# Kernel tuning notes

Hardware: AMD Instinct MI355X
Metric: run time of the kernel (lower is better)

Reference implementation:

```python
import jax, jax.numpy as jnp
import numpy as np
from jax import lax

D_MODEL, D_STATE, DT_RANK = 2048, 16, 128
B_SZ, SEQLEN = 4, 2048


def setup_inputs() -> dict:
    key = jax.random.key(0)
    ks = jax.random.split(key, 8)
    dt_init_std = DT_RANK ** (-0.5)
    return {
        "hidden_states": jax.random.normal(ks[0], (B_SZ, SEQLEN, D_MODEL), jnp.float32),
        "x_proj_weight": jax.random.normal(ks[1], (DT_RANK + 2 * D_STATE, D_MODEL), jnp.float32) * (D_MODEL ** -0.5),
        "dt_proj_weight": jax.random.uniform(ks[2], (D_MODEL, DT_RANK), jnp.float32, -dt_init_std, dt_init_std),
        "dt_proj_bias": jax.random.normal(ks[3], (D_MODEL,), jnp.float32) * 0.5 - 4.0,  # ~inv-softplus of small dt
        "A_log": jnp.log(jax.random.uniform(ks[4], (D_MODEL, D_STATE), jnp.float32) * D_STATE + 1.0),
        "D": jax.random.uniform(ks[5], (D_MODEL,), jnp.float32) * 0.8,
        "out_proj_weight": jax.random.normal(ks[6], (D_MODEL, D_MODEL), jnp.float32) * (D_MODEL ** -0.5),
        "out_proj_bias": jax.random.normal(ks[7], (D_MODEL,), jnp.float32) * 0.02,
    }


def _s6_forward(hidden_states, x_proj_weight, dt_proj_weight, dt_proj_bias,
                A_log, D, out_proj_weight, out_proj_bias):
    b, L, d = hidden_states.shape
    W = x_proj_weight.T                                   # [d, r+2n]
    r = dt_proj_weight.shape[1]
    n = (W.shape[1] - r) // 2
    dt_down = W[:, :r]                                    # [d, r]
    WB = W[:, r:r + n]                                    # [d, n]
    WC = W[:, r + n:]                                     # [d, n]

    Bm = jnp.einsum('bld,dn->bln', hidden_states, WB)     # [b, L, n]
    Cm = jnp.einsum('bld,dn->bln', hidden_states, WC)     # [b, L, n]
    dt_w = dt_proj_weight @ dt_down.T                     # [d, d] fused dt projection
    dt = jnp.einsum('bld,ed->ble', hidden_states, dt_w)   # [b, L, d]

    A = -jnp.exp(A_log)                                   # [d, n]
    delta = jax.nn.softplus(dt + dt_proj_bias)            # [b, L, d]

    def step(h, inp):
        delta_t, B_t, C_t, x_t = inp                      # [b,d],[b,n],[b,n],[b,d]
        dA = jnp.exp(delta_t[..., None] * A)              # [b, d, n]
        h = h * dA + (delta_t * x_t)[..., None] * B_t[:, None, :]
        y_t = jnp.einsum('bdn,bn->bd', h, C_t)
        return h, y_t

    h0 = jnp.zeros((b, d, n), hidden_states.dtype)
    xs = (delta.transpose(1, 0, 2), Bm.transpose(1, 0, 2),
          Cm.transpose(1, 0, 2), hidden_states.transpose(1, 0, 2))
    _, ys = lax.scan(step, h0, xs)                        # ys: [L, b, d]
    y = ys.transpose(1, 0, 2)                             # [b, L, d]

    out = jax.nn.relu(y @ out_proj_weight.T + out_proj_bias)
    out = out + D * hidden_states                         # theory mode: D applied post-relu
    return out


def reference(hidden_states, x_proj_weight, dt_proj_weight, dt_proj_bias,
              A_log, D, out_proj_weight, out_proj_bias):
    return _s6_forward(hidden_states, x_proj_weight, dt_proj_weight, dt_proj_bias,
                       A_log, D, out_proj_weight, out_proj_bias)
```

## Files before the change

kernel.cpp:

```cpp
#include <hip/hip_runtime.h>
#include <hip/hip_bf16.h>
#include <stdint.h>

#define D_MODEL 2048
#define D_STATE 16
#define DT_RANK 128
#define B_SZ 4
#define SEQLEN 2048
#define MROWS (B_SZ * SEQLEN)
#define NPROJ (DT_RANK + 2 * D_STATE)
#define NCHUNK 32
#define CHUNK (SEQLEN / NCHUNK)

typedef short bf16x8 __attribute__((ext_vector_type(8)));
typedef unsigned short ushort8 __attribute__((ext_vector_type(8)));
typedef float f32x4 __attribute__((ext_vector_type(4)));

__device__ __forceinline__ unsigned short f2bf(float f) {
  union { float f; uint32_t u; } a; a.f = f;
  uint32_t u = a.u;
  u += 0x7fffu + ((u >> 16) & 1u);
  return (unsigned short)(u >> 16);
}
__device__ __forceinline__ float bf2f(unsigned short h) {
  union { uint32_t u; float f; } a; a.u = ((uint32_t)h) << 16;
  return a.f;
}

__device__ __forceinline__ void async16(const void* g, void* l) {
  __builtin_amdgcn_global_load_lds((const __attribute__((address_space(1))) void*)g,
                                   (__attribute__((address_space(3))) void*)(uintptr_t)l,
                                   16, 0, 0);
}

template<int BM, int BN, int WMv, int WNv, bool A_BF, bool B_BF, int EPI>
__global__ __launch_bounds__(256)
void gemm_nt(const float* __restrict__ Af, const unsigned short* __restrict__ Ab,
             const float* __restrict__ Bf, const unsigned short* __restrict__ Bb,
             int K,
             float* __restrict__ outf, unsigned short* __restrict__ outb,
             const float* __restrict__ bias, const float* __restrict__ Dvec,
             const float* __restrict__ hsres)
{
  constexpr int TM = BM / WMv, TN = BN / WNv;
  constexpr int FM = TM / 16, FN = TN / 16;
  __shared__ char smem[(BM + BN) * 64];
  char* smA = smem;
  char* smB = smem + BM * 64;

  const int tid  = threadIdx.x;
  const int lane = tid & 63;
  const int wid  = tid >> 6;
  const int wm   = wid / WNv, wn = wid % WNv;
  const int wrow = wm * TM,  wcol = wn * TN;
  const int row0 = blockIdx.x * BM;
  const int col0 = blockIdx.y * BN;

  f32x4 acc[FM][FN] = {};

  for (int k0 = 0; k0 < K; k0 += 32) {
    if constexpr (A_BF) {
      #pragma unroll
      for (int it = 0; it < (BM * 4) / 256; ++it) {
        int c = it * 256 + tid;
        const char* g = (const char*)(Ab + (size_t)(row0 + (c >> 2)) * K + k0) + (c & 3) * 16;
        async16(g, smA + it * 4096 + (tid & ~63) * 16);
      }
    } else {
      constexpr int CH = BM * 4;
      #pragma unroll
      for (int it = 0; it < (CH + 255) / 256; ++it) {
        int c = it * 256 + tid;
        if ((CH % 256 == 0) || (c < CH)) {
          const float* g = Af + (size_t)(row0 + (c >> 2)) * K + k0 + (c & 3) * 8;
          float4 u = *reinterpret_cast<const float4*>(g);
          float4 v = *reinterpret_cast<const float4*>(g + 4);
          ushort8 p;
          p[0] = f2bf(u.x); p[1] = f2bf(u.y); p[2] = f2bf(u.z); p[3] = f2bf(u.w);
          p[4] = f2bf(v.x); p[5] = f2bf(v.y); p[6] = f2bf(v.z); p[7] = f2bf(v.w);
          *reinterpret_cast<ushort8*>(smA + c * 16) = p;
        }
      }
    }
    if constexpr (B_BF) {
      #pragma unroll
      for (int it = 0; it < (BN * 4) / 256; ++it) {
        int c = it * 256 + tid;
        const char* g = (const char*)(Bb + (size_t)(col0 + (c >> 2)) * K + k0) + (c & 3) * 16;
        async16(g, smB + it * 4096 + (tid & ~63) * 16);
      }
    } else {
      constexpr int CH = BN * 4;
      #pragma unroll
      for (int it = 0; it < (CH + 255) / 256; ++it) {
        int c = it * 256 + tid;
        if ((CH % 256 == 0) || (c < CH)) {
          const float* g = Bf + (size_t)(col0 + (c >> 2)) * K + k0 + (c & 3) * 8;
          float4 u = *reinterpret_cast<const float4*>(g);
          float4 v = *reinterpret_cast<const float4*>(g + 4);
          ushort8 p;
          p[0] = f2bf(u.x); p[1] = f2bf(u.y); p[2] = f2bf(u.z); p[3] = f2bf(u.w);
          p[4] = f2bf(v.x); p[5] = f2bf(v.y); p[6] = f2bf(v.z); p[7] = f2bf(v.w);
          *reinterpret_cast<ushort8*>(smB + c * 16) = p;
        }
      }
    }
    __syncthreads();

    bf16x8 a[FM], b[FN];
    const int kb = (lane >> 4) * 16;
    #pragma unroll
    for (int i = 0; i < FM; ++i)
      a[i] = *reinterpret_cast<const bf16x8*>(smA + (wrow + i * 16 + (lane & 15)) * 64 + kb);
    #pragma unroll
    for (int j = 0; j < FN; ++j)
      b[j] = *reinterpret_cast<const bf16x8*>(smB + (wcol + j * 16 + (lane & 15)) * 64 + kb);
    #pragma unroll
    for (int i = 0; i < FM; ++i)
      #pragma unroll
      for (int j = 0; j < FN; ++j)
        acc[i][j] = __builtin_amdgcn_mfma_f32_16x16x32_bf16(a[i], b[j], acc[i][j], 0, 0, 0);
    __syncthreads();
  }

  #pragma unroll
  for (int i = 0; i < FM; ++i) {
    #pragma unroll
    for (int j = 0; j < FN; ++j) {
      #pragma unroll
      for (int r = 0; r < 4; ++r) {
        int grow = row0 + wrow + i * 16 + ((lane >> 4) * 4) + r;
        int gcol = col0 + wcol + j * 16 + (lane & 15);
        float v = acc[i][j][r];
        if constexpr (EPI == 0) {
          outf[(size_t)grow * NPROJ + gcol] = v;
          if (gcol < DT_RANK) outb[(size_t)grow * DT_RANK + gcol] = f2bf(v);
        } else if constexpr (EPI == 1) {
          float s = v + bias[gcol];
          s = (s > 20.f) ? s : log1pf(__expf(s));
          outb[(size_t)grow * D_MODEL + gcol] = f2bf(s);
        } else {
          float s = fmaxf(v + bias[gcol], 0.f)
                    + Dvec[gcol] * hsres[(size_t)grow * D_MODEL + gcol];
          outf[(size_t)grow * D_MODEL + gcol] = s;
        }
      }
    }
  }
}

template<bool P2>
__global__ __launch_bounds__(256)
void scan_chunk(const unsigned short* __restrict__ delta,
                const float* __restrict__ hs,
                const float* __restrict__ xdbc,
                const float* __restrict__ A_log,
                float* __restrict__ Ssum, float* __restrict__ Hloc,
                const float* __restrict__ Hinit,
                unsigned short* __restrict__ y)
{
  const int b  = blockIdx.z;
  const int c  = blockIdx.y;
  const int d  = blockIdx.x * 256 + threadIdx.x;
  const int t0 = c * CHUNK;
  __shared__ float Bs[CHUNK][16];
  __shared__ float Cs[P2 ? CHUNK : 1][16];

  {
    int tt = threadIdx.x >> 2, nn = (threadIdx.x & 3) * 4;
    const float* src = xdbc + (size_t)(b * SEQLEN + t0 + tt) * NPROJ + DT_RANK;
    *reinterpret_cast<float4*>(&Bs[tt][nn]) = *reinterpret_cast<const float4*>(src + nn);
    if constexpr (P2)
      *reinterpret_cast<float4*>(&Cs[tt][nn]) = *reinterpret_cast<const float4*>(src + D_STATE + nn);
  }

  float A[16], h[16];
  #pragma unroll
  for (int n = 0; n < 16; ++n) A[n] = -__expf(A_log[d * 16 + n]);
  const size_t hoff = ((size_t)((b * NCHUNK + c) * D_MODEL) + d) * 16;
  if constexpr (P2) {
    #pragma unroll
    for (int n = 0; n < 16; ++n) h[n] = Hinit[hoff + n];
  } else {
    #pragma unroll
    for (int n = 0; n < 16; ++n) h[n] = 0.f;
  }
  __syncthreads();

  float S = 0.f;
  const size_t rbase = (size_t)(b * SEQLEN + t0) * D_MODEL + d;
  #pragma unroll 2
  for (int t = 0; t < CHUNK; ++t) {
    float dlt = bf2f(delta[rbase + (size_t)t * D_MODEL]);
    float x   = hs[rbase + (size_t)t * D_MODEL];
    float dx  = dlt * x;
    S += dlt;
    float yv = 0.f;
    #pragma unroll
    for (int n = 0; n < 16; ++n) {
      float dA = __expf(dlt * A[n]);
      h[n] = fmaf(h[n], dA, dx * Bs[t][n]);
      if constexpr (P2) yv = fmaf(h[n], Cs[t][n], yv);
    }
    if constexpr (P2) y[rbase + (size_t)t * D_MODEL] = f2bf(yv);
  }

  if constexpr (!P2) {
    Ssum[(size_t)((b * NCHUNK + c) * D_MODEL) + d] = S;
    #pragma unroll
    for (int n = 0; n < 16; ++n) Hloc[hoff + n] = h[n];
  }
}

__global__ __launch_bounds__(256)
void scan_prop(const float* __restrict__ A_log, const float* __restrict__ Ssum,
               const float* __restrict__ Hloc, float* __restrict__ Hinit)
{
  int idx = blockIdx.x * 256 + threadIdx.x;
  int n = idx & 15, d = (idx >> 4) & (D_MODEL - 1), b = idx >> 15;
  float A = -__expf(A_log[d * D_STATE + n]);
  float H = 0.f;
  for (int c = 0; c < NCHUNK; ++c) {
    size_t off = ((size_t)((b * NCHUNK + c) * D_MODEL) + d) * 16 + n;
    Hinit[off] = H;
    float P = __expf(A * Ssum[(size_t)((b * NCHUNK + c) * D_MODEL) + d]);
    H = fmaf(H, P, Hloc[off]);
  }
}

__global__ __launch_bounds__(256)
void cast_kernel(const float* __restrict__ in, unsigned short* __restrict__ out)
{
  int i = (blockIdx.x * 256 + threadIdx.x) * 8;
  float4 u = *reinterpret_cast<const float4*>(in + i);
  float4 v = *reinterpret_cast<const float4*>(in + i + 4);
  ushort8 p;
  p[0] = f2bf(u.x); p[1] = f2bf(u.y); p[2] = f2bf(u.z); p[3] = f2bf(u.w);
  p[4] = f2bf(v.x); p[5] = f2bf(v.y); p[6] = f2bf(v.z); p[7] = f2bf(v.w);
  *reinterpret_cast<ushort8*>(out + i) = p;
}

extern "C" void kernel_launch(void* const* d_in, const int* in_sizes, int n_in,
                              void* d_out, int out_size, void* d_ws, size_t ws_size,
                              hipStream_t stream)
{
  const float* hs   = (const float*)d_in[0];
  const float* xpw  = (const float*)d_in[1];
  const float* dtw  = (const float*)d_in[2];
  const float* dtb  = (const float*)d_in[3];
  const float* Alog = (const float*)d_in[4];
  const float* Dv   = (const float*)d_in[5];
  const float* opw  = (const float*)d_in[6];
  const float* opb  = (const float*)d_in[7];
  float* out = (float*)d_out;

  char* ws = (char*)d_ws;
  float*          xdbc  = (float*)(ws);
  unsigned short* dtmp  = (unsigned short*)(ws + 5242880);
  unsigned short* delta = (unsigned short*)(ws + 7340032);
  unsigned short* ybf   = (unsigned short*)(ws + 40894464);
  unsigned short* w3b   = (unsigned short*)(ws + 74448896);
  float*          Hloc  = (float*)(ws + 82837504);
  float*          Hinit = (float*)(ws + 99614720);
  float*          Ssum  = (float*)(ws + 116391936);

  cast_kernel<<<dim3((D_MODEL * D_MODEL) / (256 * 8)), 256, 0, stream>>>(opw, w3b);

  gemm_nt<64, 32, 2, 2, false, false, 0>
      <<<dim3(MROWS / 64, NPROJ / 32), 256, 0, stream>>>(
      hs, nullptr, xpw, nullptr, D_MODEL, xdbc, dtmp, nullptr, nullptr, nullptr);

  gemm_nt<128, 128, 2, 2, true, false, 1>
      <<<dim3(MROWS / 128, D_MODEL / 128), 256, 0, stream>>>(
      nullptr, dtmp, dtw, nullptr, DT_RANK, nullptr, delta, dtb, nullptr, nullptr);

  scan_chunk<false><<<dim3(D_MODEL / 256, NCHUNK, B_SZ), 256, 0, stream>>>(
      delta, hs, xdbc, Alog, Ssum, Hloc, nullptr, nullptr);
  scan_prop<<<dim3((B_SZ * D_MODEL * D_STATE) / 256), 256, 0, stream>>>(
      Alog, Ssum, Hloc, Hinit);
  scan_chunk<true><<<dim3(D_MODEL / 256, NCHUNK, B_SZ), 256, 0, stream>>>(
      delta, hs, xdbc, Alog, nullptr, nullptr, Hinit, ybf);

  gemm_nt<128, 128, 2, 2, true, true, 2>
      <<<dim3(MROWS / 128, D_MODEL / 128), 256, 0, stream>>>(
      nullptr, ybf, nullptr, w3b, D_MODEL, out, nullptr, opb, Dv, hs);

  (void)in_sizes; (void)n_in; (void)out_size; (void)ws_size;
}
```

Before: 491.6 us.

## Add triple-buffered 256x128 async-LDS GEMM for dt and out projections

Adds a new gemm_big kernel with 512 threads, 256x128 tiles, K-step 64, a three-stage async global-to-LDS pipeline, an XOR-swizzled LDS layout and a grouped block-index swizzle. It is used for the dt-projection and out-projection GEMMs. The x_proj and dt_proj weights are now pre-cast to bf16, and the x_proj GEMM becomes a single 160-wide column tile that loads bf16 B through async loads. The aim is to overlap memory latency with MFMA work and cut LDS bank conflicts, at the cost of more LDS per block and extra cast launches.

```diff
diff --git a/kernel.cpp b/kernel.cpp
--- a/kernel.cpp
+++ b/kernel.cpp
@@ -33,14 +33,119 @@
                                    16, 0, 0);
 }
 
+template<int EPI>
+__global__ __launch_bounds__(512, 2)
+void gemm_big(const unsigned short* __restrict__ A, const unsigned short* __restrict__ B,
+              int K,
+              float* __restrict__ outf, unsigned short* __restrict__ outb,
+              const float* __restrict__ bias, const float* __restrict__ Dvec,
+              const float* __restrict__ hsres)
+{
+  __shared__ char lds[3 * 49152];
+
+  const int tid  = threadIdx.x;
+  const int lane = tid & 63;
+  const int wid  = tid >> 6;
+  const int wrow = (wid >> 1) * 64;
+  const int wcol = (wid & 1) * 64;
+  const int nwg = gridDim.x;
+  const int cpx = nwg >> 3;
+  const int swz = (blockIdx.x & 7) * cpx + (blockIdx.x >> 3);
+  const int mb  = swz >> 4;
+  const int nb  = swz & 15;
+  const int row0 = mb * 256;
+  const int col0 = nb * 128;
+
+  const int nt = K >> 6;
+
+  auto stage_tile = [&](int t, int q) {
+    const int k0 = t * 64;
+    char* bufA = lds + q * 49152;
+    char* bufB = bufA + 32768;
+    #pragma unroll
+    for (int it = 0; it < 4; ++it) {
+      int c = it * 512 + tid;
+      int gc = c ^ ((c >> 3) & 7);
+      const char* g = (const char*)(A + (size_t)(row0 + (gc >> 3)) * K + k0) + (gc & 7) * 16;
+      async16(g, bufA + (c & ~63) * 16);
+    }
+    #pragma unroll
+    for (int it = 0; it < 2; ++it) {
+      int c = it * 512 + tid;
+      int gc = c ^ ((c >> 3) & 7);
+      const char* g = (const char*)(B + (size_t)(col0 + (gc >> 3)) * K + k0) + (gc & 7) * 16;
+      async16(g, bufB + (c & ~63) * 16);
+    }
+  };
+
+  f32x4 acc[4][4] = {};
+
+  stage_tile(0, 0);
+  stage_tile(1, 1);
+
+  for (int t = 0; t < nt; ++t) {
+    if (t < nt - 1) asm volatile("s_waitcnt vmcnt(6)" ::: "memory");
+    else            asm volatile("s_waitcnt vmcnt(0)" ::: "memory");
+    __builtin_amdgcn_s_barrier();
+    if (t + 2 < nt) stage_tile(t + 2, (t + 2) % 3);
+
+    const char* bufA = lds + (t % 3) * 49152;
+    const char* bufB = bufA + 32768;
+    #pragma unroll
+    for (int kk = 0; kk < 2; ++kk) {
+      bf16x8 a[4], b[4];
+      #pragma unroll
+      for (int i = 0; i < 4; ++i) {
+        int r = wrow + i * 16 + (lane & 15);
+        int byt = r * 128 + kk * 64 + ((lane >> 4) * 16);
+        a[i] = *reinterpret_cast<const bf16x8*>(bufA + (byt ^ ((r & 7) << 4)));
+      }
+      #pragma unroll
+      for (int j = 0; j < 4; ++j) {
+        int r = wcol + j * 16 + (lane & 15);
+        int byt = r * 128 + kk * 64 + ((lane >> 4) * 16);
+        b[j] = *reinterpret_cast<const bf16x8*>(bufB + (byt ^ ((r & 7) << 4)));
+      }
+      __builtin_amdgcn_s_setprio(1);
+      #pragma unroll
+      for (int i = 0; i < 4; ++i)
+        #pragma unroll
+        for (int j = 0; j < 4; ++j)
+          acc[i][j] = __builtin_amdgcn_mfma_f32_16x16x32_bf16(a[i], b[j], acc[i][j], 0, 0, 0);
+      __builtin_amdgcn_s_setprio(0);
+    }
+  }
+
+  #pragma unroll
+  for (int i = 0; i < 4; ++i) {
+    #pragma unroll
+    for (int j = 0; j < 4; ++j) {
+      #pragma unroll
+      for (int r = 0; r < 4; ++r) {
+        int grow = row0 + wrow + i * 16 + ((lane >> 4) * 4) + r;
+        int gcol = col0 + wcol + j * 16 + (lane & 15);
+        float v = acc[i][j][r];
+        if constexpr (EPI == 1) {
+          float s = v + bias[gcol];
+          s = (s > 20.f) ? s : log1pf(__expf(s));
+          outb[(size_t)grow * D_MODEL + gcol] = f2bf(s);
+        } else {
+          float s = fmaxf(v + bias[gcol], 0.f)
+                    + Dvec[gcol] * hsres[(size_t)grow * D_MODEL + gcol];
+          outf[(size_t)grow * D_MODEL + gcol] = s;
+        }
+      }
+    }
+  }
+}
+
 template<int BM, int BN, int WMv, int WNv, bool A_BF, bool B_BF, int EPI>
 __global__ __launch_bounds__(256)
 void gemm_nt(const float* __restrict__ Af, const unsigned short* __restrict__ Ab,
              const float* __restrict__ Bf, const unsigned short* __restrict__ Bb,
              int K,
              float* __restrict__ outf, unsigned short* __restrict__ outb,
-             const float* __restrict__ bias, const float* __restrict__ Dvec,
-             const float* __restrict__ hsres)
+             const float* __restrict__ bias)
 {
   constexpr int TM = BM / WMv, TN = BN / WNv;
   constexpr int FM = TM / 16, FN = TN / 16;
@@ -59,49 +164,45 @@
   f32x4 acc[FM][FN] = {};
 
   for (int k0 = 0; k0 < K; k0 += 32) {
-    if constexpr (A_BF) {
-      #pragma unroll
-      for (int it = 0; it < (BM * 4) / 256; ++it) {
-        int c = it * 256 + tid;
-        const char* g = (const char*)(Ab + (size_t)(row0 + (c >> 2)) * K + k0) + (c & 3) * 16;
-        async16(g, smA + it * 4096 + (tid & ~63) * 16);
-      }
-    } else {
+    {
       constexpr int CH = BM * 4;
       #pragma unroll
       for (int it = 0; it < (CH + 255) / 256; ++it) {
         int c = it * 256 + tid;
         if ((CH % 256 == 0) || (c < CH)) {
-          const float* g = Af + (size_t)(row0 + (c >> 2)) * K + k0 + (c & 3) * 8;
-          float4 u = *reinterpret_cast<const float4*>(g);
-          float4 v = *reinterpret_cast<const float4*>(g + 4);
-          ushort8 p;
-          p[0] = f2bf(u.x); p[1] = f2bf(u.y); p[2] = f2bf(u.z); p[3] = f2bf(u.w);
-          p[4] = f2bf(v.x); p[5] = f2bf(v.y); p[6] = f2bf(v.z); p[7] = f2bf(v.w);
-          *reinterpret_cast<ushort8*>(smA + c * 16) = p;
+          if constexpr (A_BF) {
+            const char* g = (const char*)(Ab + (size_t)(row0 + (c >> 2)) * K + k0) + (c & 3) * 16;
+            async16(g, smA + (c & ~63) * 16);
+          } else {
+            const float* g = Af + (size_t)(row0 + (c >> 2)) * K + k0 + (c & 3) * 8;
+            float4 u = *reinterpret_cast<const float4*>(g);
+            float4 v = *reinterpret_cast<const float4*>(g + 4);
+            ushort8 p;
+            p[0] = f2bf(u.x); p[1] = f2bf(u.y); p[2] = f2bf(u.z); p[3] = f2bf(u.w);
+            p[4] = f2bf(v.x); p[5] = f2bf(v.y); p[6] = f2bf(v.z); p[7] = f2bf(v.w);
+            *reinterpret_cast<ushort8*>(smA + c * 16) = p;
+          }
         }
       }
     }
-    if constexpr (B_BF) {
-      #pragma unroll
-      for (int it = 0; it < (BN * 4) / 256; ++it) {
-        int c = it * 256 + tid;
-        const char* g = (const char*)(Bb + (size_t)(col0 + (c >> 2)) * K + k0) + (c & 3) * 16;
-        async16(g, smB + it * 4096 + (tid & ~63) * 16);
-      }
-    } else {
+    {
       constexpr int CH = BN * 4;
       #pragma unroll
       for (int it = 0; it < (CH + 255) / 256; ++it) {
         int c = it * 256 + tid;
         if ((CH % 256 == 0) || (c < CH)) {
-          const float* g = Bf + (size_t)(col0 + (c >> 2)) * K + k0 + (c & 3) * 8;
-          float4 u = *reinterpret_cast<const float4*>(g);
-          float4 v = *reinterpret_cast<const float4*>(g + 4);
-          ushort8 p;
-          p[0] = f2bf(u.x); p[1] = f2bf(u.y); p[2] = f2bf(u.z); p[3] = f2bf(u.w);
-          p[4] = f2bf(v.x); p[5] = f2bf(v.y); p[6] = f2bf(v.z); p[7] = f2bf(v.w);
-          *reinterpret_cast<ushort8*>(smB + c * 16) = p;
+          if constexpr (B_BF) {
+            const char* g = (const char*)(Bb + (size_t)(col0 + (c >> 2)) * K + k0) + (c & 3) * 16;
+            async16(g, smB + (c & ~63) * 16);
+          } else {
+            const float* g = Bf + (size_t)(col0 + (c >> 2)) * K + k0 + (c & 3) * 8;
+            float4 u = *reinterpret_cast<const float4*>(g);
+            float4 v = *reinterpret_cast<const float4*>(g + 4);
+            ushort8 p;
+            p[0] = f2bf(u.x); p[1] = f2bf(u.y); p[2] = f2bf(u.z); p[3] = f2bf(u.w);
+            p[4] = f2bf(v.x); p[5] = f2bf(v.y); p[6] = f2bf(v.z); p[7] = f2bf(v.w);
+            *reinterpret_cast<ushort8*>(smB + c * 16) = p;
+          }
         }
       }
     }
@@ -135,14 +236,10 @@
         if constexpr (EPI == 0) {
           outf[(size_t)grow * NPROJ + gcol] = v;
           if (gcol < DT_RANK) outb[(size_t)grow * DT_RANK + gcol] = f2bf(v);
-        } else if constexpr (EPI == 1) {
+        } else {
           float s = v + bias[gcol];
           s = (s > 20.f) ? s : log1pf(__expf(s));
           outb[(size_t)grow * D_MODEL + gcol] = f2bf(s);
-        } else {
-          float s = fmaxf(v + bias[gcol], 0.f)
-                    + Dvec[gcol] * hsres[(size_t)grow * D_MODEL + gcol];
-          outf[(size_t)grow * D_MODEL + gcol] = s;
         }
       }
     }
@@ -263,16 +360,19 @@
   float*          Hloc  = (float*)(ws + 82837504);
   float*          Hinit = (float*)(ws + 99614720);
   float*          Ssum  = (float*)(ws + 116391936);
-
-  cast_kernel<<<dim3((D_MODEL * D_MODEL) / (256 * 8)), 256, 0, stream>>>(opw, w3b);
-
-  gemm_nt<64, 32, 2, 2, false, false, 0>
-      <<<dim3(MROWS / 64, NPROJ / 32), 256, 0, stream>>>(
-      hs, nullptr, xpw, nullptr, D_MODEL, xdbc, dtmp, nullptr, nullptr, nullptr);
-
-  gemm_nt<128, 128, 2, 2, true, false, 1>
-      <<<dim3(MROWS / 128, D_MODEL / 128), 256, 0, stream>>>(
-      nullptr, dtmp, dtw, nullptr, DT_RANK, nullptr, delta, dtb, nullptr, nullptr);
+  unsigned short* xpwb  = (unsigned short*)(ws + 117440512);
+  unsigned short* dtwb  = (unsigned short*)(ws + 118095872);
+
+  cast_kernel<<<dim3((D_MODEL * D_MODEL) / 2048), 256, 0, stream>>>(opw, w3b);
+  cast_kernel<<<dim3((NPROJ * D_MODEL) / 2048), 256, 0, stream>>>(xpw, xpwb);
+  cast_kernel<<<dim3((D_MODEL * DT_RANK) / 2048), 256, 0, stream>>>(dtw, dtwb);
+
+  gemm_nt<64, 160, 2, 2, false, true, 0>
+      <<<dim3(MROWS / 64, 1), 256, 0, stream>>>(
+      hs, nullptr, nullptr, xpwb, D_MODEL, xdbc, dtmp, nullptr);
+
+  gemm_big<1><<<dim3(512), 512, 0, stream>>>(
+      dtmp, dtwb, DT_RANK, nullptr, delta, dtb, nullptr, nullptr);
 
   scan_chunk<false><<<dim3(D_MODEL / 256, NCHUNK, B_SZ), 256, 0, stream>>>(
       delta, hs, xdbc, Alog, Ssum, Hloc, nullptr, nullptr);
@@ -281,9 +381,8 @@
   scan_chunk<true><<<dim3(D_MODEL / 256, NCHUNK, B_SZ), 256, 0, stream>>>(
       delta, hs, xdbc, Alog, nullptr, nullptr, Hinit, ybf);
 
-  gemm_nt<128, 128, 2, 2, true, true, 2>
-      <<<dim3(MROWS / 128, D_MODEL / 128), 256, 0, stream>>>(
-      nullptr, ybf, nullptr, w3b, D_MODEL, out, nullptr, opb, Dv, hs);
+  gemm_big<2><<<dim3(512), 512, 0, stream>>>(
+      ybf, w3b, D_MODEL, out, nullptr, opb, Dv, hs);
 
   (void)in_sizes; (void)n_in; (void)out_size; (void)ws_size;
 }
```

New measurement: 474.3 us. -3.5%, faster.

## Pre-cast projection weights to bf16 and add dedicated K=128 dt-projection GEMM

Applied to the files above, without the earlier changes.

Casts x_proj and dt_proj weights to bf16 up front so the GEMMs load them with async global-to-LDS copies instead of converting fp32 on the fly. The x_proj GEMM now uses a 32x160 tile covering all projection columns, so hidden_states is read once instead of five times. The dt projection gets a specialised kernel that loads the full K=128 slice into XOR-swizzled LDS at once and uses a branch-free fast softplus. This adds two small cast launches and uses a larger LDS footprint per block.

```diff
diff --git a/kernel.cpp b/kernel.cpp
--- a/kernel.cpp
+++ b/kernel.cpp
@@ -33,6 +33,82 @@
                                    16, 0, 0);
 }
 
+__device__ __forceinline__ float softplus_fast(float s) {
+  float e = __expf(-fabsf(s));
+  return fmaxf(s, 0.f) + __logf(1.f + e);
+}
+
+__global__ __launch_bounds__(256)
+void gemm_k128(const unsigned short* __restrict__ A, const unsigned short* __restrict__ B,
+               unsigned short* __restrict__ outb, const float* __restrict__ bias)
+{
+  __shared__ char smA[128 * 256];
+  __shared__ char smB[128 * 256];
+
+  const int tid  = threadIdx.x;
+  const int lane = tid & 63;
+  const int wid  = tid >> 6;
+  const int wrow = (wid >> 1) * 64;
+  const int wcol = (wid & 1) * 64;
+  const int row0 = blockIdx.x * 128;
+  const int col0 = blockIdx.y * 128;
+
+  #pragma unroll
+  for (int it = 0; it < 8; ++it) {
+    int c = it * 256 + tid;
+    int gc = c ^ ((c >> 4) & 7);
+    async16((const char*)(A + (size_t)(row0 + (gc >> 4)) * DT_RANK) + (gc & 15) * 16,
+            smA + (c & ~63) * 16);
+  }
+  #pragma unroll
+  for (int it = 0; it < 8; ++it) {
+    int c = it * 256 + tid;
+    int gc = c ^ ((c >> 4) & 7);
+    async16((const char*)(B + (size_t)(col0 + (gc >> 4)) * DT_RANK) + (gc & 15) * 16,
+            smB + (c & ~63) * 16);
+  }
+  __syncthreads();
+
+  f32x4 acc[4][4] = {};
+  #pragma unroll
+  for (int kk = 0; kk < 4; ++kk) {
+    bf16x8 a[4], b[4];
+    #pragma unroll
+    for (int i = 0; i < 4; ++i) {
+      int r = wrow + i * 16 + (lane & 15);
+      int byt = r * 256 + kk * 64 + ((lane >> 4) * 16);
+      a[i] = *reinterpret_cast<const bf16x8*>(smA + (byt ^ ((r & 7) << 4)));
+    }
+    #pragma unroll
+    for (int j = 0; j < 4; ++j) {
+      int r = wcol + j * 16 + (lane & 15);
+      int byt = r * 256 + kk * 64 + ((lane >> 4) * 16);
+      b[j] = *reinterpret_cast<const bf16x8*>(smB + (byt ^ ((r & 7) << 4)));
+    }
+    #pragma unroll
+    for (int i = 0; i < 4; ++i)
+      #pragma unroll
+      for (int j = 0; j < 4; ++j)
+        acc[i][j] = __builtin_amdgcn_mfma_f32_16x16x32_bf16(a[i], b[j], acc[i][j], 0, 0, 0);
+  }
+
+  float sbias[4];
+  #pragma unroll
+  for (int j = 0; j < 4; ++j) sbias[j] = bias[col0 + wcol + j * 16 + (lane & 15)];
+  #pragma unroll
+  for (int i = 0; i < 4; ++i) {
+    #pragma unroll
+    for (int j = 0; j < 4; ++j) {
+      #pragma unroll
+      for (int r = 0; r < 4; ++r) {
+        int grow = row0 + wrow + i * 16 + ((lane >> 4) * 4) + r;
+        int gcol = col0 + wcol + j * 16 + (lane & 15);
+        outb[(size_t)grow * D_MODEL + gcol] = f2bf(softplus_fast(acc[i][j][r] + sbias[j]));
+      }
+    }
+  }
+}
+
 template<int BM, int BN, int WMv, int WNv, bool A_BF, bool B_BF, int EPI>
 __global__ __launch_bounds__(256)
 void gemm_nt(const float* __restrict__ Af, const unsigned short* __restrict__ Ab,
@@ -59,49 +135,45 @@
   f32x4 acc[FM][FN] = {};
 
   for (int k0 = 0; k0 < K; k0 += 32) {
-    if constexpr (A_BF) {
-      #pragma unroll
-      for (int it = 0; it < (BM * 4) / 256; ++it) {
-        int c = it * 256 + tid;
-        const char* g = (const char*)(Ab + (size_t)(row0 + (c >> 2)) * K + k0) + (c & 3) * 16;
-        async16(g, smA + it * 4096 + (tid & ~63) * 16);
-      }
-    } else {
+    {
       constexpr int CH = BM * 4;
       #pragma unroll
       for (int it = 0; it < (CH + 255) / 256; ++it) {
         int c = it * 256 + tid;
         if ((CH % 256 == 0) || (c < CH)) {
-          const float* g = Af + (size_t)(row0 + (c >> 2)) * K + k0 + (c & 3) * 8;
-          float4 u = *reinterpret_cast<const float4*>(g);
-          float4 v = *reinterpret_cast<const float4*>(g + 4);
-          ushort8 p;
-          p[0] = f2bf(u.x); p[1] = f2bf(u.y); p[2] = f2bf(u.z); p[3] = f2bf(u.w);
-          p[4] = f2bf(v.x); p[5] = f2bf(v.y); p[6] = f2bf(v.z); p[7] = f2bf(v.w);
-          *reinterpret_cast<ushort8*>(smA + c * 16) = p;
+          if constexpr (A_BF) {
+            const char* g = (const char*)(Ab + (size_t)(row0 + (c >> 2)) * K + k0) + (c & 3) * 16;
+            async16(g, smA + (c & ~63) * 16);
+          } else {
+            const float* g = Af + (size_t)(row0 + (c >> 2)) * K + k0 + (c & 3) * 8;
+            float4 u = *reinterpret_cast<const float4*>(g);
+            float4 v = *reinterpret_cast<const float4*>(g + 4);
+            ushort8 p;
+            p[0] = f2bf(u.x); p[1] = f2bf(u.y); p[2] = f2bf(u.z); p[3] = f2bf(u.w);
+            p[4] = f2bf(v.x); p[5] = f2bf(v.y); p[6] = f2bf(v.z); p[7] = f2bf(v.w);
+            *reinterpret_cast<ushort8*>(smA + c * 16) = p;
+          }
         }
       }
     }
-    if constexpr (B_BF) {
-      #pragma unroll
-      for (int it = 0; it < (BN * 4) / 256; ++it) {
-        int c = it * 256 + tid;
-        const char* g = (const char*)(Bb + (size_t)(col0 + (c >> 2)) * K + k0) + (c & 3) * 16;
-        async16(g, smB + it * 4096 + (tid & ~63) * 16);
-      }
-    } else {
+    {
       constexpr int CH = BN * 4;
       #pragma unroll
       for (int it = 0; it < (CH + 255) / 256; ++it) {
         int c = it * 256 + tid;
         if ((CH % 256 == 0) || (c < CH)) {
-          const float* g = Bf + (size_t)(col0 + (c >> 2)) * K + k0 + (c & 3) * 8;
-          float4 u = *reinterpret_cast<const float4*>(g);
-          float4 v = *reinterpret_cast<const float4*>(g + 4);
-          ushort8 p;
-          p[0] = f2bf(u.x); p[1] = f2bf(u.y); p[2] = f2bf(u.z); p[3] = f2bf(u.w);
-          p[4] = f2bf(v.x); p[5] = f2bf(v.y); p[6] = f2bf(v.z); p[7] = f2bf(v.w);
-          *reinterpret_cast<ushort8*>(smB + c * 16) = p;
+          if constexpr (B_BF) {
+            const char* g = (const char*)(Bb + (size_t)(col0 + (c >> 2)) * K + k0) + (c & 3) * 16;
+            async16(g, smB + (c & ~63) * 16);
+          } else {
+            const float* g = Bf + (size_t)(col0 + (c >> 2)) * K + k0 + (c & 3) * 8;
+            float4 u = *reinterpret_cast<const float4*>(g);
+            float4 v = *reinterpret_cast<const float4*>(g + 4);
+            ushort8 p;
+            p[0] = f2bf(u.x); p[1] = f2bf(u.y); p[2] = f2bf(u.z); p[3] = f2bf(u.w);
+            p[4] = f2bf(v.x); p[5] = f2bf(v.y); p[6] = f2bf(v.z); p[7] = f2bf(v.w);
+            *reinterpret_cast<ushort8*>(smB + c * 16) = p;
+          }
         }
       }
     }
@@ -135,10 +207,6 @@
         if constexpr (EPI == 0) {
           outf[(size_t)grow * NPROJ + gcol] = v;
           if (gcol < DT_RANK) outb[(size_t)grow * DT_RANK + gcol] = f2bf(v);
-        } else if constexpr (EPI == 1) {
-          float s = v + bias[gcol];
-          s = (s > 20.f) ? s : log1pf(__expf(s));
-          outb[(size_t)grow * D_MODEL + gcol] = f2bf(s);
         } else {
           float s = fmaxf(v + bias[gcol], 0.f)
                     + Dvec[gcol] * hsres[(size_t)grow * D_MODEL + gcol];
@@ -263,16 +331,19 @@
   float*          Hloc  = (float*)(ws + 82837504);
   float*          Hinit = (float*)(ws + 99614720);
   float*          Ssum  = (float*)(ws + 116391936);
-
-  cast_kernel<<<dim3((D_MODEL * D_MODEL) / (256 * 8)), 256, 0, stream>>>(opw, w3b);
-
-  gemm_nt<64, 32, 2, 2, false, false, 0>
-      <<<dim3(MROWS / 64, NPROJ / 32), 256, 0, stream>>>(
-      hs, nullptr, xpw, nullptr, D_MODEL, xdbc, dtmp, nullptr, nullptr, nullptr);
-
-  gemm_nt<128, 128, 2, 2, true, false, 1>
-      <<<dim3(MROWS / 128, D_MODEL / 128), 256, 0, stream>>>(
-      nullptr, dtmp, dtw, nullptr, DT_RANK, nullptr, delta, dtb, nullptr, nullptr);
+  unsigned short* xpwb  = (unsigned short*)(ws + 117440512);
+  unsigned short* dtwb  = (unsigned short*)(ws + 118095872);
+
+  cast_kernel<<<dim3((D_MODEL * D_MODEL) / 2048), 256, 0, stream>>>(opw, w3b);
+  cast_kernel<<<dim3((NPROJ * D_MODEL) / 2048), 256, 0, stream>>>(xpw, xpwb);
+  cast_kernel<<<dim3((D_MODEL * DT_RANK) / 2048), 256, 0, stream>>>(dtw, dtwb);
+
+  gemm_nt<32, 160, 2, 2, false, true, 0>
+      <<<dim3(MROWS / 32, 1), 256, 0, stream>>>(
+      hs, nullptr, nullptr, xpwb, D_MODEL, xdbc, dtmp, nullptr, nullptr, nullptr);
+
+  gemm_k128<<<dim3(MROWS / 128, D_MODEL / 128), 256, 0, stream>>>(
+      dtmp, dtwb, delta, dtb);
 
   scan_chunk<false><<<dim3(D_MODEL / 256, NCHUNK, B_SZ), 256, 0, stream>>>(
       delta, hs, xdbc, Alog, Ssum, Hloc, nullptr, nullptr);
```

Measured after the change: 440.4 us. 10.4% less time.
